# Optimization experiments

Hardware: AMD Instinct MI355X
Metric: run time of the kernel (lower is better)

The kernel has to match this reference:

```python
import jax, jax.numpy as jnp
import numpy as np

B, S, D, H, E = 2, 512, 768, 12, 8
FF = 4 * D
HD = D // H


def setup_inputs() -> dict:
    key = jax.random.key(0)
    ks = jax.random.split(key, 12)
    s = 0.02
    return {
        "x": jax.random.normal(ks[0], (B, S, D), jnp.float32),
        "ln1_g": jnp.ones((D,), jnp.float32),
        "ln1_b": jnp.zeros((D,), jnp.float32),
        "ln2_g": jnp.ones((D,), jnp.float32),
        "ln2_b": jnp.zeros((D,), jnp.float32),
        "in_proj_w": jax.random.normal(ks[1], (3 * D, D), jnp.float32) * s,
        "in_proj_b": jax.random.normal(ks[2], (3 * D,), jnp.float32) * s,
        "out_proj_w": jax.random.normal(ks[3], (D, D), jnp.float32) * s,
        "out_proj_b": jax.random.normal(ks[4], (D,), jnp.float32) * s,
        "router_w": jax.random.normal(ks[5], (E, D), jnp.float32) * s,
        "router_b": jax.random.normal(ks[6], (E,), jnp.float32) * s,
        "w1": jax.random.normal(ks[7], (E, D, FF), jnp.float32) * s,
        "b1": jax.random.normal(ks[8], (E, FF), jnp.float32) * s,
        "w2": jax.random.normal(ks[9], (E, FF, D), jnp.float32) * s,
        "b2": jax.random.normal(ks[10], (E, D), jnp.float32) * s,
    }


def _layernorm(x, g, b, eps=1e-5):
    mu = x.mean(-1, keepdims=True)
    var = ((x - mu) ** 2).mean(-1, keepdims=True)
    return (x - mu) * jax.lax.rsqrt(var + eps) * g + b


def _forward(x, ln1_g, ln1_b, ln2_g, ln2_b, in_proj_w, in_proj_b,
             out_proj_w, out_proj_b, router_w, router_b, w1, b1, w2, b2):
    # --- self-attention sublayer (pre-norm per torch module ordering) ---
    h = _layernorm(x, ln1_g, ln1_b)
    qkv = h @ in_proj_w.T + in_proj_b                     # [B,S,3D]
    q, k, v = jnp.split(qkv, 3, axis=-1)
    to_heads = lambda t: t.reshape(B, S, H, HD).transpose(0, 2, 1, 3)  # [B,H,S,hd]
    q, k, v = to_heads(q), to_heads(k), to_heads(v)
    scores = jnp.einsum('bhqd,bhkd->bhqk', q, k) / np.float32(np.sqrt(HD))
    attn = jax.nn.softmax(scores, axis=-1)
    o = jnp.einsum('bhqk,bhkd->bhqd', attn, v).transpose(0, 2, 1, 3).reshape(B, S, D)
    o = o @ out_proj_w.T + out_proj_b
    x = x + o
    # --- MoE sublayer: top-2 routing, renormalized gates ---
    h2 = _layernorm(x, ln2_g, ln2_b)
    t = h2.reshape(-1, D)                                  # [T,D]
    logits = t @ router_w.T + router_b                     # [T,E]
    probs = jax.nn.softmax(logits, axis=-1)
    top_v, top_i = jax.lax.top_k(probs, 2)                 # [T,2]
    top_v = top_v / top_v.sum(-1, keepdims=True)
    # per-(token, expert) combine weight (0 if expert not in token's top-2)
    comb = jnp.sum(jax.nn.one_hot(top_i, E, dtype=probs.dtype) * top_v[..., None], axis=1)  # [T,E]
    # dense grouped-FFN: every token through every expert, zero-weighted combine
    hid = jax.nn.gelu(jnp.einsum('td,edf->tef', t, w1) + b1, approximate=False)  # exact GELU as torch
    y = jnp.einsum('tef,efd->ted', hid, w2) + b2           # [T,E,D]
    moe = jnp.einsum('te,ted->td', comb, y).reshape(B, S, D)
    return x + moe


def reference(x, ln1_g, ln1_b, ln2_g, ln2_b, in_proj_w, in_proj_b,
              out_proj_w, out_proj_b, router_w, router_b, w1, b1, w2, b2):
    return _forward(x, ln1_g, ln1_b, ln2_g, ln2_b, in_proj_w, in_proj_b,
                    out_proj_w, out_proj_b, router_w, router_b, w1, b1, w2, b2)
```

## Files before the change

### kernel.cpp

```cpp
#include <hip/hip_runtime.h>
#include <hip/hip_bf16.h>

#define BATCH 2
#define SEQ 512
#define DIM 768
#define HEADS 12
#define NEXP 8
#define FFDIM 3072
#define HDIM 64
#define NTOK (BATCH*SEQ)
#define NENT (2*NTOK)
#define YPS ((long)NENT * DIM)

typedef __hip_bfloat16 bf16;
typedef __attribute__((ext_vector_type(8))) short s8v;
typedef __attribute__((ext_vector_type(4))) float f4v;

typedef __attribute__((address_space(1))) const unsigned char gas_u8;
typedef __attribute__((address_space(3))) unsigned char las_u8;
__device__ __forceinline__ void gload16(const void* g, void* l) {
    __builtin_amdgcn_global_load_lds((gas_u8*)g, (las_u8*)l, 16, 0, 0);
}

__device__ __forceinline__ float bfbits2f(unsigned hi16) {
    union { unsigned u; float f; } c; c.u = hi16; return c.f;
}

__global__ __launch_bounds__(256) void ln_kernel(const float* __restrict__ x,
                                                 const float* __restrict__ g,
                                                 const float* __restrict__ b,
                                                 float* __restrict__ outf,
                                                 bf16* __restrict__ outb) {
    int t = blockIdx.x;
    const float* xr = x + (long)t * DIM;
    int tid = threadIdx.x;
    float v0 = xr[tid], v1 = xr[tid + 256], v2 = xr[tid + 512];
    float s = v0 + v1 + v2;
    __shared__ float red[4];
    #pragma unroll
    for (int o = 32; o; o >>= 1) s += __shfl_xor(s, o);
    if ((tid & 63) == 0) red[tid >> 6] = s;
    __syncthreads();
    s = red[0] + red[1] + red[2] + red[3];
    float mu = s * (1.f / DIM);
    float d0 = v0 - mu, d1 = v1 - mu, d2 = v2 - mu;
    float q = d0*d0 + d1*d1 + d2*d2;
    __shared__ float red2[4];
    #pragma unroll
    for (int o = 32; o; o >>= 1) q += __shfl_xor(q, o);
    if ((tid & 63) == 0) red2[tid >> 6] = q;
    __syncthreads();
    q = red2[0] + red2[1] + red2[2] + red2[3];
    float rstd = rsqrtf(q * (1.f / DIM) + 1e-5f);
    float o0 = d0 * rstd * g[tid]       + b[tid];
    float o1 = d1 * rstd * g[tid + 256] + b[tid + 256];
    float o2 = d2 * rstd * g[tid + 512] + b[tid + 512];
    if (outf) {
        float* of = outf + (long)t * DIM;
        of[tid] = o0; of[tid + 256] = o1; of[tid + 512] = o2;
    }
    if (outb) {
        bf16* ob = outb + (long)t * DIM;
        ob[tid] = __float2bfloat16(o0);
        ob[tid + 256] = __float2bfloat16(o1);
        ob[tid + 512] = __float2bfloat16(o2);
    }
}

template<int WM, int WN, bool GROUPED, bool GELU, int OUTMODE>
__global__ __launch_bounds__(256) void mfma_gemm(
    const bf16* __restrict__ A, const bf16* __restrict__ B,
    const float* __restrict__ bias, const float* __restrict__ resid,
    void* __restrict__ Cv,
    int M, int N, int K, int lda, int ldb, int ldc,
    int zdiv, int ksplit,
    long a_hi, long a_lo, long b_hi, long b_lo, long c_hi, long c_lo,
    long bias_stride, const int* __restrict__ grp_off, float alpha)
{
    constexpr int BM = 32 * WM, BN = 32 * WN;
    constexpr int ACH = BM * 4;
    constexpr int BCH = BN * 4;

    int z = blockIdx.z;
    int ze = z / ksplit, ks = z % ksplit;
    int kper = K / ksplit;
    long aoff, boff, coff;
    int m_count = M;
    if (GROUPED) {
        int m0 = grp_off[ze], m1 = grp_off[ze + 1];
        m_count = m1 - m0;
        if ((int)blockIdx.y * BM >= m_count) return;
        aoff = (long)m0 * lda;
        coff = (long)m0 * ldc;
        boff = (long)ze * b_hi;
    } else {
        int zh = ze / zdiv, zl = ze % zdiv;
        aoff = zh * a_hi + zl * a_lo;
        boff = zh * b_hi + zl * b_lo;
        coff = zh * c_hi + zl * c_lo;
    }
    const short* Ag = (const short*)(A + aoff);
    const short* Bg = (const short*)(B + boff);
    const float* biasp = bias ? bias + (long)ze * bias_stride : nullptr;
    float* Cf = (float*)Cv + coff;
    bf16*  Cb = (bf16*)Cv + coff;

    __shared__ short As[BM * 32];
    __shared__ short Bs[BN * 32];

    int tid = threadIdx.x;
    int wv = tid >> 6, ln = tid & 63;
    int wr = wv >> 1, wc = wv & 1;
    int fr = ln & 15, fq = ln >> 4;
    int bm = blockIdx.y * BM, bn = blockIdx.x * BN;

    f4v acc[WM][WN] = {};

    for (int k0 = ks * kper; k0 < (ks + 1) * kper; k0 += 32) {
        #pragma unroll
        for (int is = 0; is < ACH / 256; ++is) {
            int c = is * 256 + wv * 64 + ln;
            int m = c >> 2, kq = c & 3;
            gload16(Ag + (long)(bm + m) * lda + k0 + kq * 8,
                    &As[(is * 256 + wv * 64) * 8]);
        }
        if constexpr (ACH % 256) {
            if (tid < ACH % 256) {
                int c = (ACH / 256) * 256 + tid;
                int m = c >> 2, kq = c & 3;
                gload16(Ag + (long)(bm + m) * lda + k0 + kq * 8,
                        &As[((ACH / 256) * 256 + wv * 64) * 8]);
            }
        }
        #pragma unroll
        for (int is = 0; is < BCH / 256; ++is) {
            int c = is * 256 + wv * 64 + ln;
            int m = c >> 2, kq = c & 3;
            gload16(Bg + (long)(bn + m) * ldb + k0 + kq * 8,
                    &Bs[(is * 256 + wv * 64) * 8]);
        }
        if constexpr (BCH % 256) {
            if (tid < BCH % 256) {
                int c = (BCH / 256) * 256 + tid;
                int m = c >> 2, kq = c & 3;
                gload16(Bg + (long)(bn + m) * ldb + k0 + kq * 8,
                        &Bs[((BCH / 256) * 256 + wv * 64) * 8]);
            }
        }
        __syncthreads();
        s8v av[WM], bv[WN];
        #pragma unroll
        for (int i = 0; i < WM; ++i)
            av[i] = *(const s8v*)&As[(wr * (WM * 16) + i * 16 + fr) * 32 + fq * 8];
        #pragma unroll
        for (int j = 0; j < WN; ++j)
            bv[j] = *(const s8v*)&Bs[(wc * (WN * 16) + j * 16 + fr) * 32 + fq * 8];
        #pragma unroll
        for (int i = 0; i < WM; ++i)
            #pragma unroll
            for (int j = 0; j < WN; ++j)
                acc[i][j] = __builtin_amdgcn_mfma_f32_16x16x32_bf16(av[i], bv[j], acc[i][j], 0, 0, 0);
        __syncthreads();
    }

    #pragma unroll
    for (int i = 0; i < WM; ++i) {
        #pragma unroll
        for (int r = 0; r < 4; ++r) {
            int row = bm + wr * (WM * 16) + i * 16 + fq * 4 + r;
            if (GROUPED && row >= m_count) continue;
            #pragma unroll
            for (int j = 0; j < WN; ++j) {
                int col = bn + wc * (WN * 16) + j * 16 + fr;
                if (col < N) {
                    float v = acc[i][j][r] * alpha;
                    if (OUTMODE == 2) {
                        atomicAdd(&Cf[(long)row * ldc + col], v);
                    } else {
                        if (biasp) v += biasp[col];
                        if (GELU) v = 0.5f * v * (1.f + erff(v * 0.70710678118654752f));
                        if (resid) v += resid[(long)row * ldc + col];
                        if (OUTMODE == 1) Cb[(long)row * ldc + col] = __float2bfloat16(v);
                        else              Cf[(long)row * ldc + col] = v;
                    }
                }
            }
        }
    }
}

template<int FM, int FN, int XT, int YCAP, int KS, bool GELU, int OUTMODE>
__global__ __launch_bounds__(256) void moe_gemm(
    const bf16* __restrict__ A, const bf16* __restrict__ B,
    const float* __restrict__ bias, void* __restrict__ Cv,
    int lda, int ldb, int ldc, int Ktot, long b_hi, long bias_stride,
    const int* __restrict__ grp_off, int N, long pstride)
{
    static_assert(OUTMODE != 1 || KS == 1, "plain bf16 store requires no split-K");
    constexpr int BM = FM * 32, BN = FN * 32;
    constexpr int GA = BM / 64;
    constexpr int GB = BN / 64;
    constexpr int G = GA + GB;

    int bid = blockIdx.x;
    int e = bid & 7;
    int r = bid >> 3;
    int xt = r % XT; r /= XT;
    int yt = r % YCAP;
    int ks = r / YCAP;
    int m0 = grp_off[e], m1 = grp_off[e + 1];
    int m_count = m1 - m0;
    int bm = yt * BM;
    if (bm >= m_count) return;
    int bn = xt * BN;
    int kper = Ktot / KS;

    const short* Ag = (const short*)A + (long)m0 * lda;
    const short* Bg = (const short*)(B + (long)e * b_hi);
    const float* biasp = bias ? bias + (long)e * bias_stride : nullptr;
    float* Cf = (float*)Cv + (long)m0 * ldc + (long)ks * pstride;
    bf16*  Cb = (bf16*)Cv + (long)m0 * ldc;

    __shared__ short As[3][BM * 32];
    __shared__ short Bs[3][BN * 32];

    int tid = threadIdx.x;
    int wv = tid >> 6, ln = tid & 63;
    int wr = wv >> 1, wc = wv & 1;
    int fr = ln & 15, fq = ln >> 4;

    f4v acc[FM][FN] = {};

    auto stage = [&](int buf, int k0) {
        #pragma unroll
        for (int is = 0; is < GA; ++is) {
            int c = is * 256 + wv * 64 + ln;
            int m = c >> 2, q = c & 3;
            int qg = q ^ ((m >> 1) & 3);
            gload16(Ag + (long)(bm + m) * lda + k0 + qg * 8,
                    &As[buf][(is * 256 + wv * 64) * 8]);
        }
        #pragma unroll
        for (int is = 0; is < GB; ++is) {
            int c = is * 256 + wv * 64 + ln;
            int n = c >> 2, q = c & 3;
            int qg = q ^ ((n >> 1) & 3);
            gload16(Bg + (long)(bn + n) * ldb + k0 + qg * 8,
                    &Bs[buf][(is * 256 + wv * 64) * 8]);
        }
    };

    int kbeg = ks * kper;
    int nit = kper / 32;
    stage(0, kbeg);
    if (nit > 1) stage(1, kbeg + 32);

    for (int it = 0; it < nit; ++it) {
        if (it + 1 < nit) asm volatile("s_waitcnt vmcnt(%0)" :: "i"(G) : "memory");
        else              asm volatile("s_waitcnt vmcnt(0)" ::: "memory");
        __builtin_amdgcn_s_barrier();
        if (it + 2 < nit) stage((it + 2) % 3, kbeg + (it + 2) * 32);
        int cur = it % 3;
        __builtin_amdgcn_s_setprio(1);
        {
            s8v av[FM], bv[FN];
            #pragma unroll
            for (int i = 0; i < FM; ++i) {
                int row = wr * (FM * 16) + i * 16 + fr;
                av[i] = *(const s8v*)&As[cur][row * 32 + (fq ^ ((row >> 1) & 3)) * 8];
            }
            #pragma unroll
            for (int j = 0; j < FN; ++j) {
                int row = wc * (FN * 16) + j * 16 + fr;
                bv[j] = *(const s8v*)&Bs[cur][row * 32 + (fq ^ ((row >> 1) & 3)) * 8];
            }
            #pragma unroll
            for (int i = 0; i < FM; ++i)
                #pragma unroll
                for (int j = 0; j < FN; ++j)
                    acc[i][j] = __builtin_amdgcn_mfma_f32_16x16x32_bf16(av[i], bv[j], acc[i][j], 0, 0, 0);
        }
        __builtin_amdgcn_s_setprio(0);
    }

    #pragma unroll
    for (int i = 0; i < FM; ++i) {
        #pragma unroll
        for (int rr = 0; rr < 4; ++rr) {
            int row = bm + wr * (FM * 16) + i * 16 + fq * 4 + rr;
            if (row >= m_count) continue;
            #pragma unroll
            for (int j = 0; j < FN; ++j) {
                int col = bn + wc * (FN * 16) + j * 16 + fr;
                float v = acc[i][j][rr];
                if (OUTMODE == 0) {
                    Cf[(long)row * ldc + col] = v;
                } else {
                    if (biasp) v += biasp[col];
                    if (GELU) v = 0.5f * v * (1.f + erff(v * 0.70710678118654752f));
                    Cb[(long)row * ldc + col] = __float2bfloat16(v);
                }
            }
        }
    }
}

__global__ __launch_bounds__(256) void softmax512b(const bf16* __restrict__ s,
                                                   bf16* __restrict__ attn) {
    long row = (long)blockIdx.x * 4 + (threadIdx.x >> 6);
    int ln = threadIdx.x & 63;
    const unsigned* p = (const unsigned*)(s + row * 512);
    uint4 v = *(const uint4*)(p + ln * 4);
    unsigned u[4] = {v.x, v.y, v.z, v.w};
    float f[8];
    #pragma unroll
    for (int j = 0; j < 4; ++j) {
        f[2*j]   = bfbits2f(u[j] << 16);
        f[2*j+1] = bfbits2f(u[j] & 0xffff0000u);
    }
    float m = f[0];
    #pragma unroll
    for (int j = 1; j < 8; ++j) m = fmaxf(m, f[j]);
    #pragma unroll
    for (int o = 32; o; o >>= 1) m = fmaxf(m, __shfl_xor(m, o));
    float e[8], ssum = 0.f;
    #pragma unroll
    for (int j = 0; j < 8; ++j) { e[j] = expf(f[j] - m); ssum += e[j]; }
    #pragma unroll
    for (int o = 32; o; o >>= 1) ssum += __shfl_xor(ssum, o);
    float inv = 1.f / ssum;
    unsigned w[4];
    #pragma unroll
    for (int j = 0; j < 4; ++j) {
        bf16 lo = __float2bfloat16(e[2*j] * inv);
        bf16 hi = __float2bfloat16(e[2*j+1] * inv);
        w[j] = ((unsigned)*(unsigned short*)&hi << 16) | *(unsigned short*)&lo;
    }
    uint4 o4; o4.x = w[0]; o4.y = w[1]; o4.z = w[2]; o4.w = w[3];
    *(uint4*)((unsigned*)(attn + row * 512) + ln * 4) = o4;
}

__global__ __launch_bounds__(256) void vt_kernel(const bf16* __restrict__ qkvb,
                                                 bf16* __restrict__ vt) {
    int st = blockIdx.x;
    int z = blockIdx.y;
    int b = z / HEADS, h = z % HEADS;
    __shared__ short tile[64][65];
    int t = threadIdx.x;
    int d = t & 63, s0 = t >> 6;
    const short* q = (const short*)qkvb;
    #pragma unroll
    for (int i = 0; i < 16; ++i) {
        int s = st * 64 + s0 + i * 4;
        tile[s0 + i * 4][d] = q[(long)(b * SEQ + s) * 2304 + 2 * DIM + h * HDIM + d];
    }
    __syncthreads();
    short* o = (short*)vt;
    #pragma unroll
    for (int i = 0; i < 16; ++i) {
        int d2 = (t >> 6) + i * 4;
        o[(long)(z * 64 + d2) * 512 + st * 64 + (t & 63)] = tile[t & 63][d2];
    }
}

__global__ __launch_bounds__(256) void wtrans_kernel(const float* __restrict__ in,
                                                     bf16* __restrict__ out,
                                                     int R, int C) {
    int z = blockIdx.z;
    long ibase = (long)z * R * C;
    int rt = blockIdx.y * 64, ct = blockIdx.x * 64;
    __shared__ float tile[64][65];
    int t = threadIdx.x;
    int c = t & 63, r0 = t >> 6;
    #pragma unroll
    for (int i = 0; i < 16; ++i)
        tile[r0 + i * 4][c] = in[ibase + (long)(rt + r0 + i * 4) * C + ct + c];
    __syncthreads();
    #pragma unroll
    for (int i = 0; i < 16; ++i) {
        int cc = r0 + i * 4;
        out[ibase + (long)(ct + cc) * R + rt + c] = __float2bfloat16(tile[c][cc]);
    }
}

__global__ __launch_bounds__(256) void cvt2_kernel(const float* __restrict__ a, long na,
                                                   const float* __restrict__ b, long nb,
                                                   bf16* __restrict__ oa,
                                                   bf16* __restrict__ ob) {
    long i = ((long)blockIdx.x * 256 + threadIdx.x) * 4;
    const float* src; bf16* dst; long idx;
    if (i < na) { src = a; dst = oa; idx = i; }
    else if (i < na + nb) { src = b; dst = ob; idx = i - na; }
    else return;
    float4 v = *(const float4*)(src + idx);
    dst[idx]     = __float2bfloat16(v.x);
    dst[idx + 1] = __float2bfloat16(v.y);
    dst[idx + 2] = __float2bfloat16(v.z);
    dst[idx + 3] = __float2bfloat16(v.w);
}

__global__ __launch_bounds__(64) void router_kernel(const float* __restrict__ t2,
                                                    const float* __restrict__ rw,
                                                    const float* __restrict__ rb,
                                                    int* __restrict__ e_sel,
                                                    float* __restrict__ w_sel) {
    int t = blockIdx.x;
    int lane = threadIdx.x;
    const float* tr = t2 + (long)t * DIM;
    float tv[12];
    #pragma unroll
    for (int i = 0; i < 12; ++i) tv[i] = tr[lane + 64 * i];
    float logits[NEXP];
    #pragma unroll
    for (int e = 0; e < NEXP; ++e) {
        const float* wr = rw + (long)e * DIM;
        float s = 0.f;
        #pragma unroll
        for (int i = 0; i < 12; ++i) s += tv[i] * wr[lane + 64 * i];
        #pragma unroll
        for (int o = 32; o; o >>= 1) s += __shfl_xor(s, o);
        logits[e] = s + rb[e];
    }
    if (lane == 0) {
        int e0 = -1, e1 = -1;
        float l0 = -1e30f, l1 = -1e30f;
        #pragma unroll
        for (int e = 0; e < NEXP; ++e) {
            float l = logits[e];
            if (l > l0) { l1 = l0; e1 = e0; l0 = l; e0 = e; }
            else if (l > l1) { l1 = l; e1 = e; }
        }
        float p1 = expf(l1 - l0);
        float inv = 1.f / (1.f + p1);
        e_sel[t * 2] = e0;  e_sel[t * 2 + 1] = e1;
        w_sel[t * 2] = inv; w_sel[t * 2 + 1] = p1 * inv;
    }
}

__global__ __launch_bounds__(1024) void build_lists(const int* __restrict__ e_sel,
                                                    int* __restrict__ entry_tok,
                                                    int* __restrict__ ent_exp,
                                                    int* __restrict__ pos,
                                                    int* __restrict__ grp_off) {
    __shared__ int cnt[NEXP];
    __shared__ int off[NEXP + 1];
    __shared__ int cur[NEXP];
    int tid = threadIdx.x;
    if (tid < NEXP) cnt[tid] = 0;
    __syncthreads();
    for (int i = tid; i < NENT; i += 1024) atomicAdd(&cnt[e_sel[i]], 1);
    __syncthreads();
    if (tid == 0) {
        off[0] = 0;
        for (int e = 0; e < NEXP; ++e) off[e + 1] = off[e] + cnt[e];
        for (int e = 0; e < NEXP; ++e) cur[e] = off[e];
    }
    __syncthreads();
    for (int i = tid; i < NENT; i += 1024) {
        int e = e_sel[i];
        int p = atomicAdd(&cur[e], 1);
        entry_tok[p] = i >> 1;
        ent_exp[p] = e;
        pos[i] = p;
    }
    if (tid < NEXP + 1) grp_off[tid] = off[tid];
}

__global__ __launch_bounds__(256) void gather_kernel(const bf16* __restrict__ t2b,
                                                     const int* __restrict__ entry_tok,
                                                     bf16* __restrict__ t2g) {
    long i = (long)blockIdx.x * 256 + threadIdx.x;
    if (i >= (long)NENT * 192) return;
    int p = (int)(i / 192), q = (int)(i % 192);
    ((uint2*)t2g)[(long)p * 192 + q] = ((const uint2*)t2b)[(long)entry_tok[p] * 192 + q];
}

__global__ __launch_bounds__(256) void prefill_x1(const float* __restrict__ x,
                                                  const float* __restrict__ out_b,
                                                  float* __restrict__ x1) {
    long i = ((long)blockIdx.x * 256 + threadIdx.x) * 4;
    if (i >= (long)NTOK * DIM) return;
    int d = (int)(i % DIM);
    float4 v = *(const float4*)(x + i);
    v.x += out_b[d]; v.y += out_b[d + 1]; v.z += out_b[d + 2]; v.w += out_b[d + 3];
    *(float4*)(x1 + i) = v;
}

__global__ __launch_bounds__(256) void combine_kernel(const float* __restrict__ x1,
                                                      const float* __restrict__ ypart,
                                                      const float* __restrict__ b2,
                                                      const int* __restrict__ pos,
                                                      const int* __restrict__ e_sel,
                                                      const float* __restrict__ wsel,
                                                      float* __restrict__ out) {
    long i = (long)blockIdx.x * 256 + threadIdx.x;
    if (i >= (long)NTOK * DIM) return;
    int t = (int)(i / DIM), d = (int)(i % DIM);
    float v = x1[i];
    #pragma unroll
    for (int s = 0; s < 2; ++s) {
        long base = (long)pos[t * 2 + s] * DIM + d;
        float y = b2[(long)e_sel[t * 2 + s] * DIM + d];
        #pragma unroll
        for (int ks = 0; ks < 4; ++ks) y += ypart[base + ks * YPS];
        v += wsel[t * 2 + s] * y;
    }
    out[i] = v;
}

extern "C" void kernel_launch(void* const* d_in, const int* in_sizes, int n_in,
                              void* d_out, int out_size, void* d_ws, size_t ws_size,
                              hipStream_t stream) {
    const float* x        = (const float*)d_in[0];
    const float* ln1_g    = (const float*)d_in[1];
    const float* ln1_b    = (const float*)d_in[2];
    const float* ln2_g    = (const float*)d_in[3];
    const float* ln2_b    = (const float*)d_in[4];
    const float* in_w     = (const float*)d_in[5];
    const float* in_b     = (const float*)d_in[6];
    const float* out_w    = (const float*)d_in[7];
    const float* out_b    = (const float*)d_in[8];
    const float* router_w = (const float*)d_in[9];
    const float* router_b = (const float*)d_in[10];
    const float* w1       = (const float*)d_in[11];
    const float* b1       = (const float*)d_in[12];
    const float* w2       = (const float*)d_in[13];
    const float* b2       = (const float*)d_in[14];
    float* out = (float*)d_out;

    const long TD = (long)NTOK * DIM;
    char* p = (char*)d_ws;
    size_t off = 0;
    auto alloc = [&](size_t bytes) -> void* {
        void* r = p + off; off += (bytes + 255) & ~(size_t)255; return r;
    };
    bf16*  h_b    = (bf16*)alloc(TD * 2);
    bf16*  in_wb  = (bf16*)alloc(2304L * 768 * 2);
    bf16*  qkv_b  = (bf16*)alloc(1024L * 2304 * 2);
    bf16*  out_wb = (bf16*)alloc(768L * 768 * 2);
    bf16*  vt_b   = (bf16*)alloc((24L * 64 + 64) * 512 * 2);
    bf16*  oat_b  = (bf16*)alloc(TD * 2);
    float* x1     = (float*)alloc(TD * 4);
    float* t2     = (float*)alloc(TD * 4);
    bf16*  t2b    = (bf16*)alloc(TD * 2);
    bf16*  t2g    = (bf16*)alloc((2048L + 256) * 768 * 2);
    bf16*  w1t    = (bf16*)alloc(8L * 3072 * 768 * 2);
    bf16*  w2t    = (bf16*)alloc(8L * 768 * 3072 * 2);
    bf16*  hid    = (bf16*)alloc((2048L + 256) * 3072 * 2);
    float* ypart  = (float*)alloc(4 * YPS * 4);
    int*   e_sel     = (int*)alloc(NENT * 4);
    float* w_sel     = (float*)alloc(NENT * 4);
    int*   entry_tok = (int*)alloc(NENT * 4);
    int*   ent_exp   = (int*)alloc(NENT * 4);
    int*   pos       = (int*)alloc(NENT * 4);
    int*   grp_off   = (int*)alloc(64);
    bf16* scores = w1t;
    bf16* attn   = (bf16*)((char*)w1t + 24L * 512 * 512 * 2);

    ln_kernel<<<NTOK, 256, 0, stream>>>(x, ln1_g, ln1_b, nullptr, h_b);
    cvt2_kernel<<<2304, 256, 0, stream>>>(in_w, 2304L * 768, out_w, 768L * 768,
                                          in_wb, out_wb);
    mfma_gemm<2, 2, false, false, 1><<<dim3(36, 16, 1), 256, 0, stream>>>(
        h_b, in_wb, in_b, nullptr, qkv_b,
        NTOK, 3 * DIM, DIM, DIM, DIM, 3 * DIM,
        1, 1, 0, 0, 0, 0, 0, 0, 0, nullptr, 1.f);
    mfma_gemm<2, 4, false, false, 1><<<dim3(4, 8, 24), 256, 0, stream>>>(
        qkv_b, qkv_b + DIM, nullptr, nullptr, scores,
        SEQ, SEQ, HDIM, 3 * DIM, 3 * DIM, SEQ,
        HEADS, 1, (long)SEQ * 3 * DIM, HDIM, (long)SEQ * 3 * DIM, HDIM,
        (long)HEADS * SEQ * SEQ, (long)SEQ * SEQ,
        0, nullptr, 0.125f);
    softmax512b<<<24 * SEQ / 4, 256, 0, stream>>>(scores, attn);
    vt_kernel<<<dim3(8, 24), 256, 0, stream>>>(qkv_b, vt_b);
    mfma_gemm<1, 2, false, false, 1><<<dim3(1, 16, 24), 256, 0, stream>>>(
        attn, vt_b, nullptr, nullptr, oat_b,
        SEQ, HDIM, SEQ, SEQ, SEQ, DIM,
        HEADS, 1, (long)HEADS * SEQ * SEQ, (long)SEQ * SEQ,
        (long)HEADS * HDIM * SEQ, (long)HDIM * SEQ,
        (long)SEQ * DIM, HDIM,
        0, nullptr, 1.f);
    prefill_x1<<<768, 256, 0, stream>>>(x, out_b, x1);
    mfma_gemm<2, 2, false, false, 2><<<dim3(12, 16, 2), 256, 0, stream>>>(
        oat_b, out_wb, nullptr, nullptr, x1,
        NTOK, DIM, DIM, DIM, DIM, DIM,
        1, 2, 0, 0, 0, 0, 0, 0, 0, nullptr, 1.f);
    ln_kernel<<<NTOK, 256, 0, stream>>>(x1, ln2_g, ln2_b, t2, t2b);
    router_kernel<<<NTOK, 64, 0, stream>>>(t2, router_w, router_b, e_sel, w_sel);
    build_lists<<<1, 1024, 0, stream>>>(e_sel, entry_tok, ent_exp, pos, grp_off);
    gather_kernel<<<1536, 256, 0, stream>>>(t2b, entry_tok, t2g);
    wtrans_kernel<<<dim3(48, 12, 8), 256, 0, stream>>>(w1, w1t, DIM, FFDIM);
    moe_gemm<4, 4, 24, 8, 1, true, 1><<<8 * 24 * 8, 256, 0, stream>>>(
        t2g, w1t, b1, hid,
        DIM, DIM, FFDIM, DIM, (long)FFDIM * DIM, FFDIM, grp_off, FFDIM, 0);
    wtrans_kernel<<<dim3(12, 48, 8), 256, 0, stream>>>(w2, w2t, FFDIM, DIM);
    moe_gemm<4, 4, 6, 8, 4, false, 0><<<8 * 6 * 8 * 4, 256, 0, stream>>>(
        hid, w2t, nullptr, ypart,
        FFDIM, FFDIM, DIM, FFDIM, (long)DIM * FFDIM, 0, grp_off, DIM, YPS);
    combine_kernel<<<3072, 256, 0, stream>>>(x1, ypart, b2, pos, e_sel, w_sel, out);
}
```

Before: 197.7 us.

## Fuse MoE token gather into GEMM, merge LN2 with residual, batch weight transposes

The separate gather kernel is removed: the first expert GEMM now looks up token rows through entry_tok and loads directly from the layernorm output. The out-projection split-K drops atomics in favour of two partial buffers, which a new fused kernel sums with x and the bias before running LayerNorm 2. prefill_x1 and the separate LN pass go away with it. The two weight-transpose launches are merged into one, cutting the number of kernel launches and intermediate round trips. The costs are per-row indirect addresses in the GEMM A loads and an extra fp32 partial buffer write and read.

```diff
diff --git a/kernel.cpp b/kernel.cpp
--- a/kernel.cpp
+++ b/kernel.cpp
@@ -29,7 +29,6 @@
 __global__ __launch_bounds__(256) void ln_kernel(const float* __restrict__ x,
                                                  const float* __restrict__ g,
                                                  const float* __restrict__ b,
-                                                 float* __restrict__ outf,
                                                  bf16* __restrict__ outb) {
     int t = blockIdx.x;
     const float* xr = x + (long)t * DIM;
@@ -52,18 +51,56 @@
     __syncthreads();
     q = red2[0] + red2[1] + red2[2] + red2[3];
     float rstd = rsqrtf(q * (1.f / DIM) + 1e-5f);
-    float o0 = d0 * rstd * g[tid]       + b[tid];
-    float o1 = d1 * rstd * g[tid + 256] + b[tid + 256];
-    float o2 = d2 * rstd * g[tid + 512] + b[tid + 512];
-    if (outf) {
-        float* of = outf + (long)t * DIM;
-        of[tid] = o0; of[tid + 256] = o1; of[tid + 512] = o2;
-    }
-    if (outb) {
-        bf16* ob = outb + (long)t * DIM;
-        ob[tid] = __float2bfloat16(o0);
-        ob[tid + 256] = __float2bfloat16(o1);
-        ob[tid + 512] = __float2bfloat16(o2);
+    bf16* ob = outb + (long)t * DIM;
+    ob[tid]       = __float2bfloat16(d0 * rstd * g[tid]       + b[tid]);
+    ob[tid + 256] = __float2bfloat16(d1 * rstd * g[tid + 256] + b[tid + 256]);
+    ob[tid + 512] = __float2bfloat16(d2 * rstd * g[tid + 512] + b[tid + 512]);
+}
+
+__global__ __launch_bounds__(256) void ln2x1_kernel(const float* __restrict__ x,
+                                                    const float* __restrict__ out_b,
+                                                    const float* __restrict__ op,
+                                                    const float* __restrict__ g,
+                                                    const float* __restrict__ b,
+                                                    float* __restrict__ x1,
+                                                    float* __restrict__ t2,
+                                                    bf16* __restrict__ t2b) {
+    int t = blockIdx.x;
+    long base = (long)t * DIM;
+    int tid = threadIdx.x;
+    const long TDl = (long)NTOK * DIM;
+    float v[3];
+    #pragma unroll
+    for (int i = 0; i < 3; ++i) {
+        long idx = base + tid + i * 256;
+        v[i] = x[idx] + out_b[tid + i * 256] + op[idx] + op[idx + TDl];
+        x1[idx] = v[i];
+    }
+    float s = v[0] + v[1] + v[2];
+    __shared__ float red[4];
+    #pragma unroll
+    for (int o = 32; o; o >>= 1) s += __shfl_xor(s, o);
+    if ((tid & 63) == 0) red[tid >> 6] = s;
+    __syncthreads();
+    s = red[0] + red[1] + red[2] + red[3];
+    float mu = s * (1.f / DIM);
+    float d[3];
+    float q = 0.f;
+    #pragma unroll
+    for (int i = 0; i < 3; ++i) { d[i] = v[i] - mu; q += d[i] * d[i]; }
+    __shared__ float red2[4];
+    #pragma unroll
+    for (int o = 32; o; o >>= 1) q += __shfl_xor(q, o);
+    if ((tid & 63) == 0) red2[tid >> 6] = q;
+    __syncthreads();
+    q = red2[0] + red2[1] + red2[2] + red2[3];
+    float rstd = rsqrtf(q * (1.f / DIM) + 1e-5f);
+    #pragma unroll
+    for (int i = 0; i < 3; ++i) {
+        long idx = base + tid + i * 256;
+        float o = d[i] * rstd * g[tid + i * 256] + b[tid + i * 256];
+        t2[idx] = o;
+        t2b[idx] = __float2bfloat16(o);
     }
 }
 
@@ -189,12 +226,13 @@
     }
 }
 
-template<int FM, int FN, int XT, int YCAP, int KS, bool GELU, int OUTMODE>
+template<int FM, int FN, int XT, int YCAP, int KS, bool GELU, int OUTMODE, bool GATHER>
 __global__ __launch_bounds__(256) void moe_gemm(
     const bf16* __restrict__ A, const bf16* __restrict__ B,
     const float* __restrict__ bias, void* __restrict__ Cv,
     int lda, int ldb, int ldc, int Ktot, long b_hi, long bias_stride,
-    const int* __restrict__ grp_off, int N, long pstride)
+    const int* __restrict__ grp_off, const int* __restrict__ entry_tok,
+    int N, long pstride)
 {
     static_assert(OUTMODE != 1 || KS == 1, "plain bf16 store requires no split-K");
     constexpr int BM = FM * 32, BN = FN * 32;
@@ -215,7 +253,7 @@
     int bn = xt * BN;
     int kper = Ktot / KS;
 
-    const short* Ag = (const short*)A + (long)m0 * lda;
+    const short* Ag = (const short*)A + (GATHER ? 0 : (long)m0 * lda);
     const short* Bg = (const short*)(B + (long)e * b_hi);
     const float* biasp = bias ? bias + (long)e * bias_stride : nullptr;
     float* Cf = (float*)Cv + (long)m0 * ldc + (long)ks * pstride;
@@ -229,6 +267,19 @@
     int wr = wv >> 1, wc = wv & 1;
     int fr = ln & 15, fq = ln >> 4;
 
+    long arow[GA];
+    #pragma unroll
+    for (int is = 0; is < GA; ++is) {
+        int c = is * 256 + wv * 64 + ln;
+        int m = c >> 2;
+        if (GATHER) {
+            int gi = m0 + bm + m;
+            arow[is] = (long)entry_tok[gi < NENT ? gi : NENT - 1] * lda;
+        } else {
+            arow[is] = (long)(bm + m) * lda;
+        }
+    }
+
     f4v acc[FM][FN] = {};
 
     auto stage = [&](int buf, int k0) {
@@ -237,7 +288,7 @@
             int c = is * 256 + wv * 64 + ln;
             int m = c >> 2, q = c & 3;
             int qg = q ^ ((m >> 1) & 3);
-            gload16(Ag + (long)(bm + m) * lda + k0 + qg * 8,
+            gload16(Ag + arow[is] + k0 + qg * 8,
                     &As[buf][(is * 256 + wv * 64) * 8]);
         }
         #pragma unroll
@@ -363,23 +414,33 @@
     }
 }
 
-__global__ __launch_bounds__(256) void wtrans_kernel(const float* __restrict__ in,
-                                                     bf16* __restrict__ out,
-                                                     int R, int C) {
-    int z = blockIdx.z;
-    long ibase = (long)z * R * C;
-    int rt = blockIdx.y * 64, ct = blockIdx.x * 64;
+__global__ __launch_bounds__(256) void wtrans2_kernel(const float* __restrict__ w1,
+                                                      bf16* __restrict__ w1t,
+                                                      const float* __restrict__ w2,
+                                                      bf16* __restrict__ w2t) {
+    int id = blockIdx.x;
+    const float* in; bf16* out; int R, C, e, ct, rt;
+    if (id < 4608) {
+        e = id / 576; int rem = id % 576; ct = rem / 12; rt = rem % 12;
+        in = w1; out = w1t; R = DIM; C = FFDIM;
+    } else {
+        id -= 4608;
+        e = id / 576; int rem = id % 576; ct = rem / 48; rt = rem % 48;
+        in = w2; out = w2t; R = FFDIM; C = DIM;
+    }
+    long ibase = (long)e * R * C;
+    int rt0 = rt * 64, ct0 = ct * 64;
     __shared__ float tile[64][65];
     int t = threadIdx.x;
     int c = t & 63, r0 = t >> 6;
     #pragma unroll
     for (int i = 0; i < 16; ++i)
-        tile[r0 + i * 4][c] = in[ibase + (long)(rt + r0 + i * 4) * C + ct + c];
+        tile[r0 + i * 4][c] = in[ibase + (long)(rt0 + r0 + i * 4) * C + ct0 + c];
     __syncthreads();
     #pragma unroll
     for (int i = 0; i < 16; ++i) {
         int cc = r0 + i * 4;
-        out[ibase + (long)(ct + cc) * R + rt + c] = __float2bfloat16(tile[c][cc]);
+        out[ibase + (long)(ct0 + cc) * R + rt0 + c] = __float2bfloat16(tile[c][cc]);
     }
 }
 
@@ -439,7 +500,6 @@
 
 __global__ __launch_bounds__(1024) void build_lists(const int* __restrict__ e_sel,
                                                     int* __restrict__ entry_tok,
-                                                    int* __restrict__ ent_exp,
                                                     int* __restrict__ pos,
                                                     int* __restrict__ grp_off) {
     __shared__ int cnt[NEXP];
@@ -460,30 +520,9 @@
         int e = e_sel[i];
         int p = atomicAdd(&cur[e], 1);
         entry_tok[p] = i >> 1;
-        ent_exp[p] = e;
         pos[i] = p;
     }
     if (tid < NEXP + 1) grp_off[tid] = off[tid];
-}
-
-__global__ __launch_bounds__(256) void gather_kernel(const bf16* __restrict__ t2b,
-                                                     const int* __restrict__ entry_tok,
-                                                     bf16* __restrict__ t2g) {
-    long i = (long)blockIdx.x * 256 + threadIdx.x;
-    if (i >= (long)NENT * 192) return;
-    int p = (int)(i / 192), q = (int)(i % 192);
-    ((uint2*)t2g)[(long)p * 192 + q] = ((const uint2*)t2b)[(long)entry_tok[p] * 192 + q];
-}
-
-__global__ __launch_bounds__(256) void prefill_x1(const float* __restrict__ x,
-                                                  const float* __restrict__ out_b,
-                                                  float* __restrict__ x1) {
-    long i = ((long)blockIdx.x * 256 + threadIdx.x) * 4;
-    if (i >= (long)NTOK * DIM) return;
-    int d = (int)(i % DIM);
-    float4 v = *(const float4*)(x + i);
-    v.x += out_b[d]; v.y += out_b[d + 1]; v.z += out_b[d + 2]; v.w += out_b[d + 3];
-    *(float4*)(x1 + i) = v;
 }
 
 __global__ __launch_bounds__(256) void combine_kernel(const float* __restrict__ x1,
@@ -540,10 +579,10 @@
     bf16*  out_wb = (bf16*)alloc(768L * 768 * 2);
     bf16*  vt_b   = (bf16*)alloc((24L * 64 + 64) * 512 * 2);
     bf16*  oat_b  = (bf16*)alloc(TD * 2);
+    float* opart  = (float*)alloc(2 * TD * 4);
     float* x1     = (float*)alloc(TD * 4);
     float* t2     = (float*)alloc(TD * 4);
-    bf16*  t2b    = (bf16*)alloc(TD * 2);
-    bf16*  t2g    = (bf16*)alloc((2048L + 256) * 768 * 2);
+    bf16*  t2b    = (bf16*)alloc((NTOK + 256L) * DIM * 2);
     bf16*  w1t    = (bf16*)alloc(8L * 3072 * 768 * 2);
     bf16*  w2t    = (bf16*)alloc(8L * 768 * 3072 * 2);
     bf16*  hid    = (bf16*)alloc((2048L + 256) * 3072 * 2);
@@ -551,13 +590,12 @@
     int*   e_sel     = (int*)alloc(NENT * 4);
     float* w_sel     = (float*)alloc(NENT * 4);
     int*   entry_tok = (int*)alloc(NENT * 4);
-    int*   ent_exp   = (int*)alloc(NENT * 4);
     int*   pos       = (int*)alloc(NENT * 4);
     int*   grp_off   = (int*)alloc(64);
     bf16* scores = w1t;
     bf16* attn   = (bf16*)((char*)w1t + 24L * 512 * 512 * 2);
 
-    ln_kernel<<<NTOK, 256, 0, stream>>>(x, ln1_g, ln1_b, nullptr, h_b);
+    ln_kernel<<<NTOK, 256, 0, stream>>>(x, ln1_g, ln1_b, h_b);
     cvt2_kernel<<<2304, 256, 0, stream>>>(in_w, 2304L * 768, out_w, 768L * 768,
                                           in_wb, out_wb);
     mfma_gemm<2, 2, false, false, 1><<<dim3(36, 16, 1), 256, 0, stream>>>(
@@ -579,22 +617,22 @@
         (long)HEADS * HDIM * SEQ, (long)HDIM * SEQ,
         (long)SEQ * DIM, HDIM,
         0, nullptr, 1.f);
-    prefill_x1<<<768, 256, 0, stream>>>(x, out_b, x1);
-    mfma_gemm<2, 2, false, false, 2><<<dim3(12, 16, 2), 256, 0, stream>>>(
-        oat_b, out_wb, nullptr, nullptr, x1,
-        NTOK, DIM, DIM, DIM, DIM, DIM,
-        1, 2, 0, 0, 0, 0, 0, 0, 0, nullptr, 1.f);
-    ln_kernel<<<NTOK, 256, 0, stream>>>(x1, ln2_g, ln2_b, t2, t2b);
+    mfma_gemm<2, 2, false, false, 0><<<dim3(12, 16, 2), 256, 0, stream>>>(
+        oat_b, out_wb, nullptr, nullptr, opart,
+        NTOK, DIM, 384, DIM, DIM, DIM,
+        2, 1, 0, 384, 0, 384, 0, TD, 0, nullptr, 1.f);
+    ln2x1_kernel<<<NTOK, 256, 0, stream>>>(x, out_b, opart, ln2_g, ln2_b,
+                                           x1, t2, t2b);
     router_kernel<<<NTOK, 64, 0, stream>>>(t2, router_w, router_b, e_sel, w_sel);
-    build_lists<<<1, 1024, 0, stream>>>(e_sel, entry_tok, ent_exp, pos, grp_off);
-    gather_kernel<<<1536, 256, 0, stream>>>(t2b, entry_tok, t2g);
-    wtrans_kernel<<<dim3(48, 12, 8), 256, 0, stream>>>(w1, w1t, DIM, FFDIM);
-    moe_gemm<4, 4, 24, 8, 1, true, 1><<<8 * 24 * 8, 256, 0, stream>>>(
-        t2g, w1t, b1, hid,
-        DIM, DIM, FFDIM, DIM, (long)FFDIM * DIM, FFDIM, grp_off, FFDIM, 0);
-    wtrans_kernel<<<dim3(12, 48, 8), 256, 0, stream>>>(w2, w2t, FFDIM, DIM);
-    moe_gemm<4, 4, 6, 8, 4, false, 0><<<8 * 6 * 8 * 4, 256, 0, stream>>>(
+    build_lists<<<1, 1024, 0, stream>>>(e_sel, entry_tok, pos, grp_off);
+    wtrans2_kernel<<<9216, 256, 0, stream>>>(w1, w1t, w2, w2t);
+    moe_gemm<4, 4, 24, 8, 1, true, 1, true><<<8 * 24 * 8, 256, 0, stream>>>(
+        t2b, w1t, b1, hid,
+        DIM, DIM, FFDIM, DIM, (long)FFDIM * DIM, FFDIM, grp_off, entry_tok,
+        FFDIM, 0);
+    moe_gemm<4, 4, 6, 8, 4, false, 0, false><<<8 * 6 * 8 * 4, 256, 0, stream>>>(
         hid, w2t, nullptr, ypart,
-        FFDIM, FFDIM, DIM, FFDIM, (long)DIM * FFDIM, 0, grp_off, DIM, YPS);
+        FFDIM, FFDIM, DIM, FFDIM, (long)DIM * FFDIM, 0, grp_off, nullptr,
+        DIM, YPS);
     combine_kernel<<<3072, 256, 0, stream>>>(x1, ypart, b2, pos, e_sel, w_sel, out);
 }
```

Result: faster. 185.9 us (-6.0%).
